# Optimization experiments

Measured on AMD Instinct MI355X. Metric: run time of the kernel, lower is better.

The kernel has to match this reference:

```python
import jax, jax.numpy as jnp
import numpy as np

B, T, H = 64, 256, 128

def setup_inputs() -> dict:
    key = jax.random.key(0)
    ks = jax.random.split(key, 10)
    s = 1.0 / np.sqrt(H)
    return {
        "x": jax.random.normal(ks[0], (B, T, 2), jnp.float32),
        "enc_output": jax.random.normal(ks[1], (B, T, H), jnp.float32),
        "h0": jax.random.normal(ks[2], (B, H), jnp.float32) * s,
        "c0": jax.random.normal(ks[3], (B, H), jnp.float32) * s,
        "W1": jax.random.normal(ks[4], (H, H), jnp.float32) * s,
        "W2": jax.random.normal(ks[5], (H, H), jnp.float32) * s,
        "V": jax.random.normal(ks[6], (H,), jnp.float32) * s,
        "Wk": jax.random.normal(ks[7], (2, 4 * H), jnp.float32) * (1.0 / np.sqrt(2.0)),
        "Wr": jax.random.normal(ks[8], (H, 4 * H), jnp.float32) * s,
        "b": jnp.zeros((4 * H,), jnp.float32),
    }


def reference(x, enc_output, h0, c0, W1, W2, V, Wk, Wr, b):
    Bb, Tt, _ = x.shape
    # Precompute W1 @ enc_output once (original recomputes it T times inside K.rnn)
    enc_proj = jnp.einsum('bth,hk->btk', enc_output, W1)  # [B,T,H]

    def lstm_cell(inp, h, c):
        # Keras LSTMCell, gate order i,f,c,o; sigmoid recurrent activation, tanh activation
        z = inp @ Wk + h @ Wr + b  # [B,4H]
        zi, zf, zg, zo = jnp.split(z, 4, axis=-1)
        i = jax.nn.sigmoid(zi)
        f = jax.nn.sigmoid(zf)
        g = jnp.tanh(zg)
        o = jax.nn.sigmoid(zo)
        c_new = f * c + i * g
        h_new = o * jnp.tanh(c_new)
        return h_new, c_new

    def step(carry, _):
        h, c, ptr = carry
        h, c = lstm_cell(ptr, h, c)
        # additive attention over all encoder steps, batched (replaces inner K.rnn)
        scores = jnp.einsum('btk,k->bt', jnp.tanh(enc_proj + (h @ W2)[:, None, :]), V)
        probs = jax.nn.softmax(scores, axis=1)  # [B,T]
        # get_pointer with rank=0: top-1 of descending argsort == argmax
        idx = jnp.argmax(probs, axis=1)  # [B]
        ptr = jnp.take_along_axis(x, idx[:, None, None], axis=1)[:, 0, :]  # [B,2]
        return (h, c, ptr), probs

    ptr0 = jnp.ones((Bb, 2), x.dtype)
    _, probs_seq = jax.lax.scan(step, (h0, c0, ptr0), None, length=Tt)  # [T,B,T]
    return jnp.transpose(probs_seq, (1, 0, 2))  # [B,T,T]
```

## Files before the change

kernel.cpp:

```cpp
#include <hip/hip_runtime.h>
#include <cstddef>

#define TT 256
#define HH 128
#define EST 132
#define SCPS 260

__device__ __forceinline__ float rdlane(float v, int l) {
  return __int_as_float(__builtin_amdgcn_readlane(__float_as_int(v), l));
}
__device__ __forceinline__ float fast_sigmoid(float x) {
  const float L2E = 1.4426950408889634f;
  float y = __builtin_amdgcn_exp2f(-x * L2E);
  return __builtin_amdgcn_rcpf(1.0f + y);
}
__device__ __forceinline__ float fast_tanh(float x) {
  const float C2 = 2.8853900817779268f;
  float y = __builtin_amdgcn_exp2f(x * C2);
  return 1.0f - 2.0f * __builtin_amdgcn_rcpf(1.0f + y);
}

__global__ __attribute__((amdgpu_flat_work_group_size(512, 512),
                          amdgpu_waves_per_eu(2, 2)))
void decoder_kernel(const float* __restrict__ x,
                    const float* __restrict__ enc_output,
                    const float* __restrict__ h0,
                    const float* __restrict__ c0,
                    const float* __restrict__ W1,
                    const float* __restrict__ W2,
                    const float* __restrict__ V,
                    const float* __restrict__ Wk,
                    const float* __restrict__ Wr,
                    const float* __restrict__ bias,
                    float* __restrict__ out)
{
  __shared__ float E[TT * EST];
  __shared__ float zpart[4 * 512];
  __shared__ float scp[8 * SCPS];
  __shared__ float hbuf[HH];

  const int u    = threadIdx.x;
  const int b    = blockIdx.x;
  const int lane = u & 63;
  const int w    = u >> 6;
  const float C2  = 2.8853900817779268f;
  const float L2E = 1.4426950408889634f;

  {
    const float* encb = enc_output + (size_t)b * TT * HH;
    const int tsub = u >> 4;
    const int ks   = (u & 15) * 8;
    for (int p = 0; p < 8; ++p) {
      const int tt = p * 32 + tsub;
      float4 a0 = {0.f, 0.f, 0.f, 0.f};
      float4 a1 = {0.f, 0.f, 0.f, 0.f};
      const float4* er4 = (const float4*)(encb + tt * HH);
      for (int j4 = 0; j4 < 32; ++j4) {
        const float4 ev = er4[j4];
        const float* w1p = W1 + (j4 * 4) * HH + ks;
        float4 wa, wb;
        wa = *(const float4*)(w1p + 0 * HH); wb = *(const float4*)(w1p + 0 * HH + 4);
        a0.x += ev.x * wa.x; a0.y += ev.x * wa.y; a0.z += ev.x * wa.z; a0.w += ev.x * wa.w;
        a1.x += ev.x * wb.x; a1.y += ev.x * wb.y; a1.z += ev.x * wb.z; a1.w += ev.x * wb.w;
        wa = *(const float4*)(w1p + 1 * HH); wb = *(const float4*)(w1p + 1 * HH + 4);
        a0.x += ev.y * wa.x; a0.y += ev.y * wa.y; a0.z += ev.y * wa.z; a0.w += ev.y * wa.w;
        a1.x += ev.y * wb.x; a1.y += ev.y * wb.y; a1.z += ev.y * wb.z; a1.w += ev.y * wb.w;
        wa = *(const float4*)(w1p + 2 * HH); wb = *(const float4*)(w1p + 2 * HH + 4);
        a0.x += ev.z * wa.x; a0.y += ev.z * wa.y; a0.z += ev.z * wa.z; a0.w += ev.z * wa.w;
        a1.x += ev.z * wb.x; a1.y += ev.z * wb.y; a1.z += ev.z * wb.z; a1.w += ev.z * wb.w;
        wa = *(const float4*)(w1p + 3 * HH); wb = *(const float4*)(w1p + 3 * HH + 4);
        a0.x += ev.w * wa.x; a0.y += ev.w * wa.y; a0.z += ev.w * wa.z; a0.w += ev.w * wa.w;
        a1.x += ev.w * wb.x; a1.y += ev.w * wb.y; a1.z += ev.w * wb.z; a1.w += ev.w * wb.w;
      }
      *(float4*)(&E[tt * EST + ks])     = a0;
      *(float4*)(&E[tt * EST + ks + 4]) = a1;
    }
  }

  const int kq = u >> 7;
  const int cs = u & 127;
  float4 wr4[32];
  #pragma unroll
  for (int i = 0; i < 32; ++i)
    wr4[i] = *(const float4*)(Wr + (32 * kq + i) * 512 + 4 * cs);
  const int m = 32 * (w & 3) + (lane & 31);
  float wkA[4], wkB[4], bbg[4];
  #pragma unroll
  for (int gg = 0; gg < 4; ++gg) {
    wkA[gg] = Wk[gg * HH + m];
    wkB[gg] = Wk[512 + gg * HH + m];
    bbg[gg] = bias[gg * HH + m];
  }
  float c = c0[b * HH + m];
  float2 xr0 = *(const float2*)(x + b * (TT * 2) + 2 * (0 * 64 + lane));
  float2 xr1 = *(const float2*)(x + b * (TT * 2) + 2 * (1 * 64 + lane));
  float2 xr2 = *(const float2*)(x + b * (TT * 2) + 2 * (2 * 64 + lane));
  float2 xr3 = *(const float2*)(x + b * (TT * 2) + 2 * (3 * 64 + lane));
  const int kk = lane & 15;
  const int jq = lane >> 4;
  float w2local[32];
  #pragma unroll
  for (int i = 0; i < 32; ++i)
    w2local[i] = W2[(32 * jq + i) * HH + 16 * w + kk];
  const float v2r = -2.0f * V[16 * w + kk];
  float vL[16];
  #pragma unroll
  for (int i = 0; i < 16; ++i) vL[i] = rdlane(v2r, i);
  float ptr0 = 1.0f, ptr1 = 1.0f;
  float svr;
  {
    float v = V[lane] + V[64 + lane];
    #pragma unroll
    for (int o = 1; o < 64; o <<= 1) v += __shfl_xor(v, o, 64);
    svr = v;
  }

  __syncthreads();

  {
    float* Er = &E[(u >> 1) * EST + 64 * (u & 1)];
    #pragma unroll
    for (int i = 0; i < 16; ++i) {
      float4 ev = *(const float4*)(Er + 4 * i);
      ev.x = __builtin_amdgcn_exp2f(ev.x * C2);
      ev.y = __builtin_amdgcn_exp2f(ev.y * C2);
      ev.z = __builtin_amdgcn_exp2f(ev.z * C2);
      ev.w = __builtin_amdgcn_exp2f(ev.w * C2);
      *(float4*)(Er + 4 * i) = ev;
    }
  }
  {
    float hA0 = h0[(size_t)b * HH + 32 * kq + (lane & 31)];
    float4 zac = {0.f, 0.f, 0.f, 0.f};
    #pragma unroll
    for (int i = 0; i < 32; ++i) {
      float hi = rdlane(hA0, i);
      zac.x += hi * wr4[i].x;
      zac.y += hi * wr4[i].y;
      zac.z += hi * wr4[i].z;
      zac.w += hi * wr4[i].w;
    }
    *(float4*)(&zpart[kq * 512 + 4 * cs]) = zac;
  }
  __syncthreads();

  float* outb = out + (size_t)b * TT * TT;

  #pragma unroll 1
  for (int step = 0; step < TT; ++step) {
    if (step > 0) {
      float4 sc = {0.f, 0.f, 0.f, 0.f};
      #pragma unroll
      for (int q = 0; q < 8; ++q) {
        float4 v = *(const float4*)(&scp[q * SCPS + 4 * lane]);
        sc.x += v.x; sc.y += v.y; sc.z += v.z; sc.w += v.w;
      }
      if (w < 4) {
        float m4 = fmaxf(fmaxf(sc.x, sc.y), fmaxf(sc.z, sc.w));
        int ttl = (sc.x == m4) ? 0 : (sc.y == m4) ? 1 : (sc.z == m4) ? 2 : 3;
        float mx = m4;
        #pragma unroll
        for (int o = 1; o < 64; o <<= 1) mx = fmaxf(mx, __shfl_xor(mx, o));
        unsigned long long bal = __ballot(m4 == mx);
        int ls  = __ffsll(bal) - 1;
        int tc  = 4 * lane + ttl;
        int tts = __builtin_amdgcn_readlane(tc, ls);
        int j   = tts >> 6;
        int ll  = tts & 63;
        float2 cand = (j == 0) ? xr0 : (j == 1) ? xr1 : (j == 2) ? xr2 : xr3;
        ptr0 = rdlane(cand.x, ll);
        ptr1 = rdlane(cand.y, ll);
      } else {
        sc.x += svr; sc.y += svr; sc.z += svr; sc.w += svr;
        float p0 = __builtin_amdgcn_exp2f((sc.x - 12.0f) * L2E);
        float p1 = __builtin_amdgcn_exp2f((sc.y - 12.0f) * L2E);
        float p2 = __builtin_amdgcn_exp2f((sc.z - 12.0f) * L2E);
        float p3 = __builtin_amdgcn_exp2f((sc.w - 12.0f) * L2E);
        float ws4 = (p0 + p1) + (p2 + p3);
        #pragma unroll
        for (int o = 1; o < 64; o <<= 1) ws4 += __shfl_xor(ws4, o);
        if ((lane >> 4) == (w - 4)) {
          float rs = __builtin_amdgcn_rcpf(ws4);
          float4 po = {p0 * rs, p1 * rs, p2 * rs, p3 * rs};
          *(float4*)(&outb[(size_t)(step - 1) * TT + 4 * lane]) = po;
        }
      }
    }
    if ((lane & 32) == 0 && w < 4) {
      float z0 = bbg[0] + ptr0 * wkA[0] + ptr1 * wkB[0];
      float z1 = bbg[1] + ptr0 * wkA[1] + ptr1 * wkB[1];
      float z2 = bbg[2] + ptr0 * wkA[2] + ptr1 * wkB[2];
      float z3 = bbg[3] + ptr0 * wkA[3] + ptr1 * wkB[3];
      #pragma unroll
      for (int q = 0; q < 4; ++q) {
        z0 += zpart[q * 512 + 0 * HH + m];
        z1 += zpart[q * 512 + 1 * HH + m];
        z2 += zpart[q * 512 + 2 * HH + m];
        z3 += zpart[q * 512 + 3 * HH + m];
      }
      float ig = fast_sigmoid(z0);
      float fg = fast_sigmoid(z1);
      float gg = fast_tanh(z2);
      float og = fast_sigmoid(z3);
      c = fg * c + ig * gg;
      hbuf[m] = og * fast_tanh(c);
    }
    __syncthreads();

    float Uk;
    {
      float cp0 = 0.0f, cp1 = 0.0f;
      const float4* h4 = (const float4*)(hbuf + 32 * jq);
      #pragma unroll
      for (int i4 = 0; i4 < 8; ++i4) {
        float4 hv = h4[i4];
        cp0 += hv.x * w2local[4 * i4 + 0];
        cp1 += hv.y * w2local[4 * i4 + 1];
        cp0 += hv.z * w2local[4 * i4 + 2];
        cp1 += hv.w * w2local[4 * i4 + 3];
      }
      float csum = cp0 + cp1;
      csum += __shfl_xor(csum, 16);
      csum += __shfl_xor(csum, 32);
      Uk = __builtin_amdgcn_exp2f(csum * C2);
    }
    {
      float uL[16];
      #pragma unroll
      for (int i = 0; i < 16; ++i) uL[i] = rdlane(Uk, i);
      #pragma unroll
      for (int tt = 0; tt < 4; ++tt) {
        const float* Er = &E[(64 * tt + lane) * EST + 16 * w];
        float4 e0 = *(const float4*)(Er + 0);
        float4 e1 = *(const float4*)(Er + 4);
        float4 e2 = *(const float4*)(Er + 8);
        float4 e3 = *(const float4*)(Er + 12);
        float a0 = 0.0f, a1 = 0.0f;
        float t0, t1, n;
        t0 = fmaf(e0.x, uL[ 0], 1.0f); t1 = fmaf(e0.y, uL[ 1], 1.0f);
        n  = fmaf(vL[ 1], t0, vL[ 0] * t1);
        a0 = fmaf(n, __builtin_amdgcn_rcpf(t0 * t1), a0);
        t0 = fmaf(e0.z, uL[ 2], 1.0f); t1 = fmaf(e0.w, uL[ 3], 1.0f);
        n  = fmaf(vL[ 3], t0, vL[ 2] * t1);
        a1 = fmaf(n, __builtin_amdgcn_rcpf(t0 * t1), a1);
        t0 = fmaf(e1.x, uL[ 4], 1.0f); t1 = fmaf(e1.y, uL[ 5], 1.0f);
        n  = fmaf(vL[ 5], t0, vL[ 4] * t1);
        a0 = fmaf(n, __builtin_amdgcn_rcpf(t0 * t1), a0);
        t0 = fmaf(e1.z, uL[ 6], 1.0f); t1 = fmaf(e1.w, uL[ 7], 1.0f);
        n  = fmaf(vL[ 7], t0, vL[ 6] * t1);
        a1 = fmaf(n, __builtin_amdgcn_rcpf(t0 * t1), a1);
        t0 = fmaf(e2.x, uL[ 8], 1.0f); t1 = fmaf(e2.y, uL[ 9], 1.0f);
        n  = fmaf(vL[ 9], t0, vL[ 8] * t1);
        a0 = fmaf(n, __builtin_amdgcn_rcpf(t0 * t1), a0);
        t0 = fmaf(e2.z, uL[10], 1.0f); t1 = fmaf(e2.w, uL[11], 1.0f);
        n  = fmaf(vL[11], t0, vL[10] * t1);
        a1 = fmaf(n, __builtin_amdgcn_rcpf(t0 * t1), a1);
        t0 = fmaf(e3.x, uL[12], 1.0f); t1 = fmaf(e3.y, uL[13], 1.0f);
        n  = fmaf(vL[13], t0, vL[12] * t1);
        a0 = fmaf(n, __builtin_amdgcn_rcpf(t0 * t1), a0);
        t0 = fmaf(e3.z, uL[14], 1.0f); t1 = fmaf(e3.w, uL[15], 1.0f);
        n  = fmaf(vL[15], t0, vL[14] * t1);
        a1 = fmaf(n, __builtin_amdgcn_rcpf(t0 * t1), a1);
        scp[w * SCPS + 64 * tt + lane] = a0 + a1;
      }
    }
    {
      const float4* h4 = (const float4*)(hbuf + 32 * kq);
      float4 zac = {0.f, 0.f, 0.f, 0.f};
      #pragma unroll
      for (int i4 = 0; i4 < 8; ++i4) {
        float4 hv = h4[i4];
        zac.x += hv.x * wr4[4 * i4 + 0].x;
        zac.y += hv.x * wr4[4 * i4 + 0].y;
        zac.z += hv.x * wr4[4 * i4 + 0].z;
        zac.w += hv.x * wr4[4 * i4 + 0].w;
        zac.x += hv.y * wr4[4 * i4 + 1].x;
        zac.y += hv.y * wr4[4 * i4 + 1].y;
        zac.z += hv.y * wr4[4 * i4 + 1].z;
        zac.w += hv.y * wr4[4 * i4 + 1].w;
        zac.x += hv.z * wr4[4 * i4 + 2].x;
        zac.y += hv.z * wr4[4 * i4 + 2].y;
        zac.z += hv.z * wr4[4 * i4 + 2].z;
        zac.w += hv.z * wr4[4 * i4 + 2].w;
        zac.x += hv.w * wr4[4 * i4 + 3].x;
        zac.y += hv.w * wr4[4 * i4 + 3].y;
        zac.z += hv.w * wr4[4 * i4 + 3].z;
        zac.w += hv.w * wr4[4 * i4 + 3].w;
      }
      *(float4*)(&zpart[kq * 512 + 4 * cs]) = zac;
    }
    __syncthreads();
  }

  if (w >= 4) {
    float4 sc = {0.f, 0.f, 0.f, 0.f};
    #pragma unroll
    for (int q = 0; q < 8; ++q) {
      float4 v = *(const float4*)(&scp[q * SCPS + 4 * lane]);
      sc.x += v.x; sc.y += v.y; sc.z += v.z; sc.w += v.w;
    }
    sc.x += svr; sc.y += svr; sc.z += svr; sc.w += svr;
    float p0 = __builtin_amdgcn_exp2f((sc.x - 12.0f) * L2E);
    float p1 = __builtin_amdgcn_exp2f((sc.y - 12.0f) * L2E);
    float p2 = __builtin_amdgcn_exp2f((sc.z - 12.0f) * L2E);
    float p3 = __builtin_amdgcn_exp2f((sc.w - 12.0f) * L2E);
    float ws4 = (p0 + p1) + (p2 + p3);
    #pragma unroll
    for (int o = 1; o < 64; o <<= 1) ws4 += __shfl_xor(ws4, o);
    if ((lane >> 4) == (w - 4)) {
      float rs = __builtin_amdgcn_rcpf(ws4);
      float4 po = {p0 * rs, p1 * rs, p2 * rs, p3 * rs};
      *(float4*)(&outb[(size_t)255 * TT + 4 * lane]) = po;
    }
  }
}

extern "C" void kernel_launch(void* const* d_in, const int* in_sizes, int n_in,
                              void* d_out, int out_size, void* d_ws, size_t ws_size,
                              hipStream_t stream) {
  (void)in_sizes; (void)n_in; (void)d_ws; (void)ws_size; (void)out_size;
  const float* x    = (const float*)d_in[0];
  const float* enc  = (const float*)d_in[1];
  const float* h0   = (const float*)d_in[2];
  const float* c0   = (const float*)d_in[3];
  const float* W1   = (const float*)d_in[4];
  const float* W2   = (const float*)d_in[5];
  const float* V    = (const float*)d_in[6];
  const float* Wk   = (const float*)d_in[7];
  const float* Wr   = (const float*)d_in[8];
  const float* bias = (const float*)d_in[9];
  float* out = (float*)d_out;

  decoder_kernel<<<64, 512, 0, stream>>>(x, enc, h0, c0, W1, W2, V, Wk, Wr, bias, out);
}
```

Before: 807.7 us.

## Use DPP reductions, LDS pointer lookup, and reorder recurrent matvec before attention

Replaces shuffle-based wave reductions with DPP row moves for the first reduction stages, and remaps the W2 partial-product lanes so the cross-lane sum becomes a quad DPP sum. The pointer gather now reads x from an LDS copy instead of four register rows plus readlanes. The Wr recurrent matvec moves ahead of the attention-score loop. The scp score accumulation is also pushed inside each branch. Together these aim to shorten the latency of the serial per-step critical path, at the cost of a small extra LDS buffer and changed lane mapping.

```diff
diff --git a/kernel.cpp b/kernel.cpp
--- a/kernel.cpp
+++ b/kernel.cpp
@@ -8,6 +8,34 @@
 
 __device__ __forceinline__ float rdlane(float v, int l) {
   return __int_as_float(__builtin_amdgcn_readlane(__float_as_int(v), l));
+}
+template<int CTRL>
+__device__ __forceinline__ float dpp_mv(float x) {
+  return __int_as_float(
+      __builtin_amdgcn_mov_dpp(__float_as_int(x), CTRL, 0xF, 0xF, true));
+}
+__device__ __forceinline__ float wave_max64(float x) {
+  x = fmaxf(x, dpp_mv<0xB1>(x));
+  x = fmaxf(x, dpp_mv<0x4E>(x));
+  x = fmaxf(x, dpp_mv<0x124>(x));
+  x = fmaxf(x, dpp_mv<0x128>(x));
+  x = fmaxf(x, __shfl_xor(x, 16));
+  x = fmaxf(x, __shfl_xor(x, 32));
+  return x;
+}
+__device__ __forceinline__ float wave_sum64(float x) {
+  x += dpp_mv<0xB1>(x);
+  x += dpp_mv<0x4E>(x);
+  x += dpp_mv<0x124>(x);
+  x += dpp_mv<0x128>(x);
+  x += __shfl_xor(x, 16);
+  x += __shfl_xor(x, 32);
+  return x;
+}
+__device__ __forceinline__ float quad_sum(float x) {
+  x += dpp_mv<0xB1>(x);
+  x += dpp_mv<0x4E>(x);
+  return x;
 }
 __device__ __forceinline__ float fast_sigmoid(float x) {
   const float L2E = 1.4426950408889634f;
@@ -38,6 +66,7 @@
   __shared__ float zpart[4 * 512];
   __shared__ float scp[8 * SCPS];
   __shared__ float hbuf[HH];
+  __shared__ float xlds[2 * TT];
 
   const int u    = threadIdx.x;
   const int b    = blockIdx.x;
@@ -75,6 +104,7 @@
       *(float4*)(&E[tt * EST + ks])     = a0;
       *(float4*)(&E[tt * EST + ks + 4]) = a1;
     }
+    xlds[u] = x[b * (TT * 2) + u];
   }
 
   const int kq = u >> 7;
@@ -92,12 +122,8 @@
     bbg[gg] = bias[gg * HH + m];
   }
   float c = c0[b * HH + m];
-  float2 xr0 = *(const float2*)(x + b * (TT * 2) + 2 * (0 * 64 + lane));
-  float2 xr1 = *(const float2*)(x + b * (TT * 2) + 2 * (1 * 64 + lane));
-  float2 xr2 = *(const float2*)(x + b * (TT * 2) + 2 * (2 * 64 + lane));
-  float2 xr3 = *(const float2*)(x + b * (TT * 2) + 2 * (3 * 64 + lane));
-  const int kk = lane & 15;
-  const int jq = lane >> 4;
+  const int kk = lane >> 2;
+  const int jq = lane & 3;
   float w2local[32];
   #pragma unroll
   for (int i = 0; i < 32; ++i)
@@ -105,14 +131,12 @@
   const float v2r = -2.0f * V[16 * w + kk];
   float vL[16];
   #pragma unroll
-  for (int i = 0; i < 16; ++i) vL[i] = rdlane(v2r, i);
+  for (int i = 0; i < 16; ++i) vL[i] = rdlane(v2r, 4 * i);
   float ptr0 = 1.0f, ptr1 = 1.0f;
   float svr;
   {
     float v = V[lane] + V[64 + lane];
-    #pragma unroll
-    for (int o = 1; o < 64; o <<= 1) v += __shfl_xor(v, o, 64);
-    svr = v;
+    svr = wave_sum64(v);
   }
 
   __syncthreads();
@@ -149,36 +173,36 @@
   #pragma unroll 1
   for (int step = 0; step < TT; ++step) {
     if (step > 0) {
-      float4 sc = {0.f, 0.f, 0.f, 0.f};
-      #pragma unroll
-      for (int q = 0; q < 8; ++q) {
-        float4 v = *(const float4*)(&scp[q * SCPS + 4 * lane]);
-        sc.x += v.x; sc.y += v.y; sc.z += v.z; sc.w += v.w;
-      }
       if (w < 4) {
+        float4 sc = {0.f, 0.f, 0.f, 0.f};
+        #pragma unroll
+        for (int q = 0; q < 8; ++q) {
+          float4 v = *(const float4*)(&scp[q * SCPS + 4 * lane]);
+          sc.x += v.x; sc.y += v.y; sc.z += v.z; sc.w += v.w;
+        }
         float m4 = fmaxf(fmaxf(sc.x, sc.y), fmaxf(sc.z, sc.w));
         int ttl = (sc.x == m4) ? 0 : (sc.y == m4) ? 1 : (sc.z == m4) ? 2 : 3;
-        float mx = m4;
-        #pragma unroll
-        for (int o = 1; o < 64; o <<= 1) mx = fmaxf(mx, __shfl_xor(mx, o));
+        float mx = wave_max64(m4);
         unsigned long long bal = __ballot(m4 == mx);
         int ls  = __ffsll(bal) - 1;
         int tc  = 4 * lane + ttl;
         int tts = __builtin_amdgcn_readlane(tc, ls);
-        int j   = tts >> 6;
-        int ll  = tts & 63;
-        float2 cand = (j == 0) ? xr0 : (j == 1) ? xr1 : (j == 2) ? xr2 : xr3;
-        ptr0 = rdlane(cand.x, ll);
-        ptr1 = rdlane(cand.y, ll);
+        const float2 pp = *(const float2*)(&xlds[2 * tts]);
+        ptr0 = pp.x;
+        ptr1 = pp.y;
       } else {
+        float4 sc = {0.f, 0.f, 0.f, 0.f};
+        #pragma unroll
+        for (int q = 0; q < 8; ++q) {
+          float4 v = *(const float4*)(&scp[q * SCPS + 4 * lane]);
+          sc.x += v.x; sc.y += v.y; sc.z += v.z; sc.w += v.w;
+        }
         sc.x += svr; sc.y += svr; sc.z += svr; sc.w += svr;
         float p0 = __builtin_amdgcn_exp2f((sc.x - 12.0f) * L2E);
         float p1 = __builtin_amdgcn_exp2f((sc.y - 12.0f) * L2E);
         float p2 = __builtin_amdgcn_exp2f((sc.z - 12.0f) * L2E);
         float p3 = __builtin_amdgcn_exp2f((sc.w - 12.0f) * L2E);
-        float ws4 = (p0 + p1) + (p2 + p3);
-        #pragma unroll
-        for (int o = 1; o < 64; o <<= 1) ws4 += __shfl_xor(ws4, o);
+        float ws4 = wave_sum64((p0 + p1) + (p2 + p3));
         if ((lane >> 4) == (w - 4)) {
           float rs = __builtin_amdgcn_rcpf(ws4);
           float4 po = {p0 * rs, p1 * rs, p2 * rs, p3 * rs};
@@ -219,15 +243,38 @@
         cp0 += hv.z * w2local[4 * i4 + 2];
         cp1 += hv.w * w2local[4 * i4 + 3];
       }
-      float csum = cp0 + cp1;
-      csum += __shfl_xor(csum, 16);
-      csum += __shfl_xor(csum, 32);
+      float csum = quad_sum(cp0 + cp1);
       Uk = __builtin_amdgcn_exp2f(csum * C2);
+    }
+    {
+      const float4* h4 = (const float4*)(hbuf + 32 * kq);
+      float4 zac = {0.f, 0.f, 0.f, 0.f};
+      #pragma unroll
+      for (int i4 = 0; i4 < 8; ++i4) {
+        float4 hv = h4[i4];
+        zac.x += hv.x * wr4[4 * i4 + 0].x;
+        zac.y += hv.x * wr4[4 * i4 + 0].y;
+        zac.z += hv.x * wr4[4 * i4 + 0].z;
+        zac.w += hv.x * wr4[4 * i4 + 0].w;
+        zac.x += hv.y * wr4[4 * i4 + 1].x;
+        zac.y += hv.y * wr4[4 * i4 + 1].y;
+        zac.z += hv.y * wr4[4 * i4 + 1].z;
+        zac.w += hv.y * wr4[4 * i4 + 1].w;
+        zac.x += hv.z * wr4[4 * i4 + 2].x;
+        zac.y += hv.z * wr4[4 * i4 + 2].y;
+        zac.z += hv.z * wr4[4 * i4 + 2].z;
+        zac.w += hv.z * wr4[4 * i4 + 2].w;
+        zac.x += hv.w * wr4[4 * i4 + 3].x;
+        zac.y += hv.w * wr4[4 * i4 + 3].y;
+        zac.z += hv.w * wr4[4 * i4 + 3].z;
+        zac.w += hv.w * wr4[4 * i4 + 3].w;
+      }
+      *(float4*)(&zpart[kq * 512 + 4 * cs]) = zac;
     }
     {
       float uL[16];
       #pragma unroll
-      for (int i = 0; i < 16; ++i) uL[i] = rdlane(Uk, i);
+      for (int i = 0; i < 16; ++i) uL[i] = rdlane(Uk, 4 * i);
       #pragma unroll
       for (int tt = 0; tt < 4; ++tt) {
         const float* Er = &E[(64 * tt + lane) * EST + 16 * w];
@@ -264,31 +311,6 @@
         scp[w * SCPS + 64 * tt + lane] = a0 + a1;
       }
     }
-    {
-      const float4* h4 = (const float4*)(hbuf + 32 * kq);
-      float4 zac = {0.f, 0.f, 0.f, 0.f};
-      #pragma unroll
-      for (int i4 = 0; i4 < 8; ++i4) {
-        float4 hv = h4[i4];
-        zac.x += hv.x * wr4[4 * i4 + 0].x;
-        zac.y += hv.x * wr4[4 * i4 + 0].y;
-        zac.z += hv.x * wr4[4 * i4 + 0].z;
-        zac.w += hv.x * wr4[4 * i4 + 0].w;
-        zac.x += hv.y * wr4[4 * i4 + 1].x;
-        zac.y += hv.y * wr4[4 * i4 + 1].y;
-        zac.z += hv.y * wr4[4 * i4 + 1].z;
-        zac.w += hv.y * wr4[4 * i4 + 1].w;
-        zac.x += hv.z * wr4[4 * i4 + 2].x;
-        zac.y += hv.z * wr4[4 * i4 + 2].y;
-        zac.z += hv.z * wr4[4 * i4 + 2].z;
-        zac.w += hv.z * wr4[4 * i4 + 2].w;
-        zac.x += hv.w * wr4[4 * i4 + 3].x;
-        zac.y += hv.w * wr4[4 * i4 + 3].y;
-        zac.z += hv.w * wr4[4 * i4 + 3].z;
-        zac.w += hv.w * wr4[4 * i4 + 3].w;
-      }
-      *(float4*)(&zpart[kq * 512 + 4 * cs]) = zac;
-    }
     __syncthreads();
   }
 
@@ -304,9 +326,7 @@
     float p1 = __builtin_amdgcn_exp2f((sc.y - 12.0f) * L2E);
     float p2 = __builtin_amdgcn_exp2f((sc.z - 12.0f) * L2E);
     float p3 = __builtin_amdgcn_exp2f((sc.w - 12.0f) * L2E);
-    float ws4 = (p0 + p1) + (p2 + p3);
-    #pragma unroll
-    for (int o = 1; o < 64; o <<= 1) ws4 += __shfl_xor(ws4, o);
+    float ws4 = wave_sum64((p0 + p1) + (p2 + p3));
     if ((lane >> 4) == (w - 4)) {
       float rs = __builtin_amdgcn_rcpf(ws4);
       float4 po = {p0 * rs, p1 * rs, p2 * rs, p3 * rs};
```

Measured after the change: 818.4 us. Within noise of the previous version (+1.3%).
